# Kernel optimization log

Measured on AMD Instinct MI355X. Metric: run time of the kernel, lower is better.

## Reference

```python
import jax, jax.numpy as jnp
import numpy as np

B, S, DIM = 4, 2048, 1024
HEADS, HD = 16, DIM // 16
HIDDEN, LEVELS = 4 * DIM, 3
LN_EPS = 1e-5


def setup_inputs() -> dict:
    key = jax.random.key(0)
    ks = jax.random.split(key, 10)
    w = lambda k, shape: (jax.random.normal(k, shape, jnp.float32) * 0.02)
    return {
        "x": jax.random.normal(ks[0], (B, S, DIM), jnp.float32),
        "Wq": w(ks[1], (DIM, DIM)),
        "Wk": w(ks[2], (DIM, DIM)),
        "Wv": w(ks[3], (DIM, DIM)),
        "Wo": w(ks[4], (DIM, DIM)),
        "ln1_g": jnp.ones((DIM,), jnp.float32),
        "ln1_b": jnp.zeros((DIM,), jnp.float32),
        "ln2_g": jnp.ones((DIM,), jnp.float32),
        "ln2_b": jnp.zeros((DIM,), jnp.float32),
        "cms_w1": w(ks[5], (LEVELS, DIM, HIDDEN)),
        "cms_b1": jnp.zeros((LEVELS, HIDDEN), jnp.float32),
        "cms_w2": w(ks[6], (LEVELS, HIDDEN, DIM)),
        "cms_b2": jnp.zeros((LEVELS, DIM), jnp.float32),
    }


def _layer_norm(x, g, b):
    m = jnp.mean(x, axis=-1, keepdims=True)
    v = jnp.var(x, axis=-1, keepdims=True)
    return (x - m) * jax.lax.rsqrt(v + LN_EPS) * g + b


def _linear_attn(h, Wq, Wk, Wv, Wo):
    # h: [B, S, DIM]; feature_map(z) = elu(z) + 1 applied to Q and K
    fm = lambda z: jax.nn.elu(z) + 1.0
    Q = fm(h @ Wq).reshape(B, S, HEADS, HD)
    K = fm(h @ Wk).reshape(B, S, HEADS, HD)
    V = (h @ Wv).reshape(B, S, HEADS, HD)
    # scan over time with fast-weight memory M_t = M_{t-1} + k_t (x) v_t
    Qs = jnp.moveaxis(Q, 1, 0)  # [S, B, H, D]
    Ks = jnp.moveaxis(K, 1, 0)
    Vs = jnp.moveaxis(V, 1, 0)

    def step(carry, qkv):
        mem, ksum = carry  # [B,H,D,D], [B,H,D]
        q, k, v = qkv      # each [B,H,D]
        mem = mem + k[..., :, None] * v[..., None, :]
        ksum = ksum + k
        num = jnp.einsum('bhde,bhd->bhe', mem, q)
        den = jnp.einsum('bhd,bhd->bh', ksum, q)[..., None] + 1e-6
        return (mem, ksum), num / den

    init = (jnp.zeros((B, HEADS, HD, HD), h.dtype),
            jnp.zeros((B, HEADS, HD), h.dtype))
    _, ys = jax.lax.scan(step, init, (Qs, Ks, Vs))  # ys: [S,B,H,D]
    out = jnp.moveaxis(ys, 0, 1).reshape(B, S, DIM)
    return out @ Wo


def _cms(h, w1, b1, w2, b2):
    # Continuum Memory System: chain of LEVELS MLPs (dim->4dim->dim).
    y = h
    for l in range(LEVELS):
        y = jax.nn.gelu(y @ w1[l] + b1[l]) @ w2[l] + b2[l]
    return y


def reference(x, Wq, Wk, Wv, Wo, ln1_g, ln1_b, ln2_g, ln2_b,
              cms_w1, cms_b1, cms_w2, cms_b2):
    x = x + _linear_attn(_layer_norm(x, ln1_g, ln1_b), Wq, Wk, Wv, Wo)
    x = x + _cms(_layer_norm(x, ln2_g, ln2_b), cms_w1, cms_b1, cms_w2, cms_b2)
    return x
```

## Files before the change

kernel.cpp:

```cpp
#include <hip/hip_runtime.h>
#include <stdint.h>
#include <math.h>

#define DIM     1024
#define HID     4096
#define SEQ     2048
#define NB      4
#define NH      16
#define HD      64
#define NCHUNK  32
#define MROWS   8192
#define QSTR    3072

typedef unsigned short ushort_t;
typedef __attribute__((ext_vector_type(8))) short bf16x8;
typedef __attribute__((ext_vector_type(4))) float f32x4;

#define OFF_H    ((size_t)0)
#define OFF_Q    ((size_t)16777216)
#define OFF_P    ((size_t)67108864)
#define OFF_KS   ((size_t)100663296)
#define OFF_X1   ((size_t)101187584)
#define OFF_WQT  ((size_t)134742016)
#define OFF_WOT  ((size_t)141033472)
#define OFF_W1T  ((size_t)143130624)
#define OFF_W2T  ((size_t)168296448)
#define OFF_HIDB OFF_Q + 16777216

__device__ __forceinline__ float b2f(ushort_t u) {
    return __uint_as_float(((unsigned int)u) << 16);
}
__device__ __forceinline__ ushort_t f2b(float f) {
    unsigned int u = __float_as_uint(f);
    u += 0x7FFFu + ((u >> 16) & 1u);
    return (ushort_t)(u >> 16);
}
__device__ __forceinline__ void unpack4(uint2 u, float* f) {
    f[0] = __uint_as_float(u.x << 16);
    f[1] = __uint_as_float(u.x & 0xffff0000u);
    f[2] = __uint_as_float(u.y << 16);
    f[3] = __uint_as_float(u.y & 0xffff0000u);
}
__device__ __forceinline__ float fast_gelu(float x) {
    const float u = x * (1.5957691216057308f + 0.07135481627f * x * x);
    const float e = exp2f(-1.4426950408889634f * u);
    return x * __builtin_amdgcn_rcpf(1.0f + e);
}
__device__ __forceinline__ float fast_elu1(float x) {
    return x > 0.0f ? x + 1.0f : exp2f(1.4426950408889634f * x);
}
__device__ __forceinline__ void ldg16(const ushort_t* g, ushort_t* l) {
    __builtin_amdgcn_global_load_lds(
        (const __attribute__((address_space(1))) void*)g,
        (__attribute__((address_space(3))) void*)l, 16, 0, 0);
}

__global__ void __launch_bounds__(256)
transpose_f32_bf16(const float* __restrict__ src, ushort_t* __restrict__ dst, int R, int C)
{
    __shared__ float t[32][33];
    const int bx = blockIdx.x * 32;
    const int by = blockIdx.y * 32;
    const int tx = threadIdx.x, ty = threadIdx.y;
    #pragma unroll
    for (int i = ty; i < 32; i += 8)
        t[i][tx] = src[(size_t)(by + i) * C + bx + tx];
    __syncthreads();
    #pragma unroll
    for (int i = ty; i < 32; i += 8)
        dst[(size_t)(bx + i) * R + by + tx] = f2b(t[tx][i]);
}

__global__ void __launch_bounds__(256)
ln_fwd(const float* __restrict__ xin, const float* __restrict__ g,
       const float* __restrict__ be, ushort_t* __restrict__ out)
{
    const int row = blockIdx.x, tid = threadIdx.x;
    const float4 f = ((const float4*)(xin + (size_t)row * DIM))[tid];
    float v[4] = {f.x, f.y, f.z, f.w};
    float s  = v[0] + v[1] + v[2] + v[3];
    float ss = v[0]*v[0] + v[1]*v[1] + v[2]*v[2] + v[3]*v[3];
    #pragma unroll
    for (int off = 32; off; off >>= 1) {
        s  += __shfl_down(s, off);
        ss += __shfl_down(ss, off);
    }
    __shared__ float red[2][4];
    const int wave = tid >> 6, lane = tid & 63;
    if (lane == 0) { red[0][wave] = s; red[1][wave] = ss; }
    __syncthreads();
    s  = red[0][0] + red[0][1] + red[0][2] + red[0][3];
    ss = red[1][0] + red[1][1] + red[1][2] + red[1][3];
    const float mean = s * (1.0f / DIM);
    const float var  = ss * (1.0f / DIM) - mean * mean;
    const float rstd = rsqrtf(var + 1e-5f);
    ushort_t o[4];
    #pragma unroll
    for (int i = 0; i < 4; i++) {
        const int col = tid * 4 + i;
        o[i] = f2b((v[i] - mean) * rstd * g[col] + be[col]);
    }
    uint2 u2;
    u2.x = (unsigned int)o[0] | ((unsigned int)o[1] << 16);
    u2.y = (unsigned int)o[2] | ((unsigned int)o[3] << 16);
    *(uint2*)(out + (size_t)row * DIM + tid * 4) = u2;
}

#define ACT_NONE 0
#define ACT_ELU1 1
#define ACT_GELU 2
#define ACT_QKV  3

template<int ACT, bool BIAS, bool RES, bool OUTF32>
__global__ void __launch_bounds__(256, 4)
gemm_bt(const ushort_t* __restrict__ A, const ushort_t* __restrict__ Bt,
        const float* __restrict__ bias, const float* __restrict__ resid,
        void* __restrict__ Cout, int M, int N, int K)
{
    __shared__ __align__(16) ushort_t As[2][128 * 32];
    __shared__ __align__(16) ushort_t Bs[2][128 * 32];
    const int tid  = threadIdx.x;
    const int wave = tid >> 6, lane = tid & 63;
    const int bm = blockIdx.x * 128, bn = blockIdx.y * 128;
    const int wm = (wave >> 1) * 64, wn = (wave & 1) * 64;
    const int srow = tid >> 2;
    const int skp  = (tid & 3) * 8;
    const int mrow = lane & 15, kq = (lane >> 4) * 8;
    const bool qkv_elu = (bn < 2048);

    f32x4 acc[4][4] = {};

    const size_t arow0 = (size_t)(bm + srow)      * K;
    const size_t arow1 = (size_t)(bm + srow + 64) * K;
    const size_t brow0 = (size_t)(bn + srow)      * K;
    const size_t brow1 = (size_t)(bn + srow + 64) * K;

    for (int kt = 0; kt < K; kt += 64) {
        __syncthreads();
        #pragma unroll
        for (int hh = 0; hh < 2; hh++) {
            const int ko = kt + hh * 32;
            ldg16(A  + arow0 + ko + skp, As[hh] + tid * 8);
            ldg16(A  + arow1 + ko + skp, As[hh] + 2048 + tid * 8);
            ldg16(Bt + brow0 + ko + skp, Bs[hh] + tid * 8);
            ldg16(Bt + brow1 + ko + skp, Bs[hh] + 2048 + tid * 8);
        }
        __syncthreads();
        #pragma unroll
        for (int hh = 0; hh < 2; hh++) {
            bf16x8 af[4], bfr[4];
            #pragma unroll
            for (int r = 0; r < 4; r++)
                af[r] = *(const bf16x8*)(As[hh] + (wm + r * 16 + mrow) * 32 + kq);
            #pragma unroll
            for (int c = 0; c < 4; c++)
                bfr[c] = *(const bf16x8*)(Bs[hh] + (wn + c * 16 + mrow) * 32 + kq);
            #pragma unroll
            for (int r = 0; r < 4; r++)
                #pragma unroll
                for (int c = 0; c < 4; c++)
                    acc[r][c] = __builtin_amdgcn_mfma_f32_16x16x32_bf16(af[r], bfr[c], acc[r][c], 0, 0, 0);
        }
    }

    const int cr = (lane >> 4) * 4;
    const int cc = lane & 15;
    #pragma unroll
    for (int r = 0; r < 4; r++) {
        #pragma unroll
        for (int c = 0; c < 4; c++) {
            const int gc = bn + wn + c * 16 + cc;
            const float bv = BIAS ? bias[gc] : 0.0f;
            #pragma unroll
            for (int j = 0; j < 4; j++) {
                const int gr = bm + wm + r * 16 + cr + j;
                float vv = acc[r][c][j] + bv;
                if (ACT == ACT_ELU1) vv = fast_elu1(vv);
                if (ACT == ACT_GELU) vv = fast_gelu(vv);
                if (ACT == ACT_QKV)  vv = qkv_elu ? fast_elu1(vv) : vv;
                const size_t oidx = (size_t)gr * N + gc;
                if (RES) vv += resid[oidx];
                if (OUTF32) ((float*)Cout)[oidx] = vv;
                else        ((ushort_t*)Cout)[oidx] = f2b(vv);
            }
        }
    }
}

__global__ void __launch_bounds__(256)
attn_phase1(const ushort_t* __restrict__ qkv,
            float* __restrict__ P, float* __restrict__ Ksum)
{
    const int c = blockIdx.x, h = blockIdx.y, b = blockIdx.z;
    __shared__ ushort_t Ks[64][68], Vs[64][68];
    const int tid = threadIdx.x;
    const size_t rowbase = (size_t)b * SEQ + c * 64;
    #pragma unroll
    for (int i = 0; i < 4; i++) {
        const int lin = tid + 256 * i;
        const int t = lin >> 4, d4 = (lin & 15) * 4;
        const size_t gidx = (rowbase + t) * QSTR + h * HD + d4;
        *(uint2*)&Ks[t][d4] = *(const uint2*)(qkv + 1024 + gidx);
        *(uint2*)&Vs[t][d4] = *(const uint2*)(qkv + 2048 + gidx);
    }
    __syncthreads();
    const int d0 = (tid >> 4) * 4, e0 = (tid & 15) * 4;
    float acc[4][4] = {};
    for (int t = 0; t < 64; t++) {
        float kf[4], vf[4];
        unpack4(*(const uint2*)&Ks[t][d0], kf);
        unpack4(*(const uint2*)&Vs[t][e0], vf);
        #pragma unroll
        for (int i = 0; i < 4; i++)
            #pragma unroll
            for (int j = 0; j < 4; j++)
                acc[i][j] += kf[i] * vf[j];
    }
    const size_t pbase = (((size_t)b * NH + h) * NCHUNK + c) * 4096;
    #pragma unroll
    for (int i = 0; i < 4; i++) {
        float4 o; o.x = acc[i][0]; o.y = acc[i][1]; o.z = acc[i][2]; o.w = acc[i][3];
        *(float4*)(P + pbase + (size_t)(d0 + i) * 64 + e0) = o;
    }
    if (tid < 64) {
        float a = 0.0f;
        for (int t = 0; t < 64; t++) a += b2f(Ks[t][tid]);
        Ksum[(((size_t)b * NH + h) * NCHUNK + c) * 64 + tid] = a;
    }
}

__global__ void __launch_bounds__(256)
attn_prefix(float* __restrict__ P, float* __restrict__ Ksum)
{
    const int bh = blockIdx.y;
    const int e  = blockIdx.x * 256 + threadIdx.x;
    const size_t base = (size_t)bh * NCHUNK * 4096 + e;
    float acc = 0.0f;
    #pragma unroll
    for (int c = 0; c < NCHUNK; c++) {
        const float t = P[base + (size_t)c * 4096];
        P[base + (size_t)c * 4096] = acc;
        acc += t;
    }
    if (blockIdx.x == 0 && threadIdx.x < 64) {
        const size_t kb = (size_t)bh * NCHUNK * 64 + threadIdx.x;
        float a = 0.0f;
        #pragma unroll
        for (int c = 0; c < NCHUNK; c++) {
            const float t = Ksum[kb + c * 64];
            Ksum[kb + c * 64] = a;
            a += t;
        }
    }
}

__global__ void __launch_bounds__(256)
attn_phase2(const ushort_t* __restrict__ qkv, const float* __restrict__ P,
            const float* __restrict__ Ksum, ushort_t* __restrict__ Out)
{
    const int c = blockIdx.x, h = blockIdx.y, b = blockIdx.z;
    const int tid = threadIdx.x;
    __shared__ ushort_t Qs[64][68], KsB[64][68], VsB[64][68];
    __shared__ float S[64][68];
    __shared__ float Mp[64][64];
    __shared__ float kp[64];
    __shared__ float partial[4][64];
    const size_t rowbase = (size_t)b * SEQ + c * 64;
    const size_t pbase = (((size_t)b * NH + h) * NCHUNK + c) * 4096;
    #pragma unroll
    for (int i = 0; i < 4; i++) {
        const int lin = tid + 256 * i;
        const int t = lin >> 4, d4 = (lin & 15) * 4;
        const size_t gidx = (rowbase + t) * QSTR + h * HD + d4;
        *(uint2*)&Qs[t][d4]  = *(const uint2*)(qkv + gidx);
        *(uint2*)&KsB[t][d4] = *(const uint2*)(qkv + 1024 + gidx);
        *(uint2*)&VsB[t][d4] = *(const uint2*)(qkv + 2048 + gidx);
        *(float4*)&Mp[t][d4] = *(const float4*)(P + pbase + lin * 4);
    }
    if (tid < 64) kp[tid] = Ksum[(((size_t)b * NH + h) * NCHUNK + c) * 64 + tid];
    __syncthreads();

    const int t0 = (tid >> 4) * 4;
    const int c0 = (tid & 15) * 4;

    {
        float accS[4][4] = {};
        for (int d4 = 0; d4 < 64; d4 += 4) {
            float qf[4][4], kf[4][4];
            #pragma unroll
            for (int i = 0; i < 4; i++) {
                unpack4(*(const uint2*)&Qs[t0 + i][d4], qf[i]);
                unpack4(*(const uint2*)&KsB[c0 + i][d4], kf[i]);
            }
            #pragma unroll
            for (int i = 0; i < 4; i++)
                #pragma unroll
                for (int j = 0; j < 4; j++)
                    #pragma unroll
                    for (int dd = 0; dd < 4; dd++)
                        accS[i][j] += qf[i][dd] * kf[j][dd];
        }
        #pragma unroll
        for (int i = 0; i < 4; i++) {
            float4 sv;
            sv.x = (c0 + 0 <= t0 + i) ? accS[i][0] : 0.0f;
            sv.y = (c0 + 1 <= t0 + i) ? accS[i][1] : 0.0f;
            sv.z = (c0 + 2 <= t0 + i) ? accS[i][2] : 0.0f;
            sv.w = (c0 + 3 <= t0 + i) ? accS[i][3] : 0.0f;
            *(float4*)&S[t0 + i][c0] = sv;
        }
    }
    __syncthreads();

    {
        const int t = tid & 63, q = tid >> 6;
        const int base = q * 16;
        float a = 0.0f;
        #pragma unroll
        for (int ii = 0; ii < 16; ii++) a += S[t][base + ii];
        #pragma unroll
        for (int d = 0; d < 16; d++) a += b2f(Qs[t][base + d]) * kp[base + d];
        partial[q][t] = a;
    }
    __syncthreads();

    float acc[4][4] = {};
    for (int ii = 0; ii < 64; ii++) {
        float vf[4];
        unpack4(*(const uint2*)&VsB[ii][c0], vf);
        #pragma unroll
        for (int i = 0; i < 4; i++) {
            const float s = S[t0 + i][ii];
            #pragma unroll
            for (int j = 0; j < 4; j++) acc[i][j] += s * vf[j];
        }
    }
    for (int d = 0; d < 64; d++) {
        const float4 mp = *(const float4*)&Mp[d][c0];
        #pragma unroll
        for (int i = 0; i < 4; i++) {
            const float qv = b2f(Qs[t0 + i][d]);
            acc[i][0] += qv * mp.x; acc[i][1] += qv * mp.y;
            acc[i][2] += qv * mp.z; acc[i][3] += qv * mp.w;
        }
    }
    #pragma unroll
    for (int i = 0; i < 4; i++) {
        const float dent = partial[0][t0 + i] + partial[1][t0 + i] +
                           partial[2][t0 + i] + partial[3][t0 + i] + 1e-6f;
        const float r = 1.0f / dent;
        ushort_t o[4];
        #pragma unroll
        for (int j = 0; j < 4; j++) o[j] = f2b(acc[i][j] * r);
        uint2 u2;
        u2.x = (unsigned int)o[0] | ((unsigned int)o[1] << 16);
        u2.y = (unsigned int)o[2] | ((unsigned int)o[3] << 16);
        *(uint2*)(Out + (rowbase + t0 + i) * DIM + h * HD + c0) = u2;
    }
}

extern "C" void kernel_launch(void* const* d_in, const int* in_sizes, int n_in,
                              void* d_out, int out_size, void* d_ws, size_t ws_size,
                              hipStream_t stream)
{
    const float* x      = (const float*)d_in[0];
    const float* Wq     = (const float*)d_in[1];
    const float* Wk     = (const float*)d_in[2];
    const float* Wv     = (const float*)d_in[3];
    const float* Wo     = (const float*)d_in[4];
    const float* ln1g   = (const float*)d_in[5];
    const float* ln1b   = (const float*)d_in[6];
    const float* ln2g   = (const float*)d_in[7];
    const float* ln2b   = (const float*)d_in[8];
    const float* cw1    = (const float*)d_in[9];
    const float* cb1    = (const float*)d_in[10];
    const float* cw2    = (const float*)d_in[11];
    const float* cb2    = (const float*)d_in[12];

    char* ws = (char*)d_ws;
    ushort_t* h     = (ushort_t*)(ws + OFF_H);
    ushort_t* qkv   = (ushort_t*)(ws + OFF_Q);
    float*    Pb    = (float*)(ws + OFF_P);
    float*    ksb   = (float*)(ws + OFF_KS);
    float*    x1    = (float*)(ws + OFF_X1);
    ushort_t* wqkvt = (ushort_t*)(ws + OFF_WQT);
    ushort_t* wot   = (ushort_t*)(ws + OFF_WOT);
    ushort_t* w1t   = (ushort_t*)(ws + OFF_W1T);
    ushort_t* w2t   = (ushort_t*)(ws + OFF_W2T);
    ushort_t* hid   = (ushort_t*)(ws + OFF_HIDB);
    float*    outp  = (float*)d_out;

    const dim3 tb(32, 8);
    transpose_f32_bf16<<<dim3(32, 32), tb, 0, stream>>>(Wq, wqkvt,                   DIM, DIM);
    transpose_f32_bf16<<<dim3(32, 32), tb, 0, stream>>>(Wk, wqkvt + 1024 * 1024,     DIM, DIM);
    transpose_f32_bf16<<<dim3(32, 32), tb, 0, stream>>>(Wv, wqkvt + 2 * 1024 * 1024, DIM, DIM);
    transpose_f32_bf16<<<dim3(32, 32), tb, 0, stream>>>(Wo, wot, DIM, DIM);
    for (int l = 0; l < 3; l++) {
        transpose_f32_bf16<<<dim3(128, 32), tb, 0, stream>>>(cw1 + (size_t)l * DIM * HID,
                                                             w1t + (size_t)l * HID * DIM, DIM, HID);
        transpose_f32_bf16<<<dim3(32, 128), tb, 0, stream>>>(cw2 + (size_t)l * HID * DIM,
                                                             w2t + (size_t)l * DIM * HID, HID, DIM);
    }

    ln_fwd<<<MROWS, 256, 0, stream>>>(x, ln1g, ln1b, h);

    gemm_bt<ACT_QKV, false, false, false><<<dim3(64, 24), 256, 0, stream>>>(
        h, wqkvt, nullptr, nullptr, qkv, MROWS, QSTR, DIM);

    attn_phase1<<<dim3(NCHUNK, NH, NB), 256, 0, stream>>>(qkv, Pb, ksb);
    attn_prefix<<<dim3(16, 64), 256, 0, stream>>>(Pb, ksb);
    attn_phase2<<<dim3(NCHUNK, NH, NB), 256, 0, stream>>>(qkv, Pb, ksb, h);

    gemm_bt<ACT_NONE, false, true, true><<<dim3(64, 8), 256, 0, stream>>>(h, wot, nullptr, x, x1, MROWS, DIM, DIM);

    ln_fwd<<<MROWS, 256, 0, stream>>>(x1, ln2g, ln2b, h);

    const ushort_t* cur = h;
    for (int l = 0; l < 3; l++) {
        gemm_bt<ACT_GELU, true, false, false><<<dim3(64, 32), 256, 0, stream>>>(
            cur, w1t + (size_t)l * HID * DIM, cb1 + (size_t)l * HID, nullptr, hid, MROWS, HID, DIM);
        if (l < 2) {
            gemm_bt<ACT_NONE, true, false, false><<<dim3(64, 8), 256, 0, stream>>>(
                hid, w2t + (size_t)l * DIM * HID, cb2 + (size_t)l * DIM, nullptr, h, MROWS, DIM, HID);
            cur = h;
        } else {
            gemm_bt<ACT_NONE, true, true, true><<<dim3(64, 8), 256, 0, stream>>>(
                hid, w2t + (size_t)l * DIM * HID, cb2 + (size_t)l * DIM, x1, outp, MROWS, DIM, HID);
        }
    }
    (void)in_sizes; (void)n_in; (void)out_size; (void)ws_size;
}
```

Baseline: 883.2 us.

## Replace 128x128 GEMM with 256-row 8-wave pipelined GEMM using swizzled LDS

Adds a new gemm256 kernel that uses 256xBN tiles, 512 threads (8 waves), and an XOR-swizzled LDS layout to avoid bank conflicts. It double-buffers global-to-LDS loads across sub-phases, interleaving stages with MFMA groups under explicit barriers and s_setprio. All GEMM launches in the transformer block are switched to it, with BN=256 for the wide FFN up-projection. This aims to raise arithmetic intensity and overlap memory with compute. The cost is much higher LDS use and register pressure, plus fewer blocks for the narrow N=1024 GEMMs (256 blocks), which may underfill the GPU.

```diff
diff --git a/kernel.cpp b/kernel.cpp
--- a/kernel.cpp
+++ b/kernel.cpp
@@ -123,13 +123,12 @@
     const int wave = tid >> 6, lane = tid & 63;
     const int bm = blockIdx.x * 128, bn = blockIdx.y * 128;
     const int wm = (wave >> 1) * 64, wn = (wave & 1) * 64;
+    const int skp  = (tid & 3) * 8;
     const int srow = tid >> 2;
-    const int skp  = (tid & 3) * 8;
     const int mrow = lane & 15, kq = (lane >> 4) * 8;
     const bool qkv_elu = (bn < 2048);
 
     f32x4 acc[4][4] = {};
-
     const size_t arow0 = (size_t)(bm + srow)      * K;
     const size_t arow1 = (size_t)(bm + srow + 64) * K;
     const size_t brow0 = (size_t)(bn + srow)      * K;
@@ -162,7 +161,6 @@
                     acc[r][c] = __builtin_amdgcn_mfma_f32_16x16x32_bf16(af[r], bfr[c], acc[r][c], 0, 0, 0);
         }
     }
-
     const int cr = (lane >> 4) * 4;
     const int cc = lane & 15;
     #pragma unroll
@@ -185,6 +183,158 @@
             }
         }
     }
+}
+
+
+#define G256_RD_A(BUF, FR0) \
+    _Pragma("unroll") for (int _i = 0; _i < 4; ++_i) \
+    _Pragma("unroll") for (int _kk = 0; _kk < 2; ++_kk) \
+        af[_i][_kk] = *(const bf16x8*)(ldsb + (BUF) + aoff + (((FR0) + _i) << 11) \
+                                       + (((_kk << 6) | qv16) ^ mflip))
+
+#define G256_RD_B(BUF, FC0, CNT) \
+    _Pragma("unroll") for (int _c = 0; _c < (CNT); ++_c) \
+    _Pragma("unroll") for (int _kk = 0; _kk < 2; ++_kk) \
+        bf[(FC0) + _c][_kk] = *(const bf16x8*)(ldsb + (BUF) + boff + (((FC0) + _c) << 11) \
+                                               + (((_kk << 6) | qv16) ^ mflip))
+
+#define G256_MFMA(AR, C0, CNT) \
+    _Pragma("unroll") for (int _i = 0; _i < 4; ++_i) \
+    _Pragma("unroll") for (int _c = 0; _c < (CNT); ++_c) \
+    _Pragma("unroll") for (int _kk = 0; _kk < 2; ++_kk) \
+        acc[(AR) + _i][(C0) + _c] = __builtin_amdgcn_mfma_f32_16x16x32_bf16( \
+            af[_i][_kk], bf[(C0) + _c][_kk], acc[(AR) + _i][(C0) + _c], 0, 0, 0)
+
+#define G256_STAGE_A(T, H) do { \
+    char* _d = ldsb + (((T) & 1) ? (int)BUFSZ : 0) + ((H) << 14) + (tid << 4); \
+    const ushort_t* _s = pA + (size_t)((H) * 128) * K + (size_t)(T) * 64; \
+    ldg16(_s, (ushort_t*)_d); \
+    ldg16(_s + (size_t)64 * K, (ushort_t*)(_d + 8192)); \
+} while (0)
+
+#define G256_STAGE_B(T, H) do { \
+    char* _d = ldsb + (((T) & 1) ? (int)BUFSZ : 0) + 32768 + (H) * (BN_ * 64) + (tid << 4); \
+    const ushort_t* _s = pB + (size_t)((H) * (BN_ >> 1)) * K + (size_t)(T) * 64; \
+    ldg16(_s, (ushort_t*)_d); \
+    if (BN_ == 256) ldg16(_s + (size_t)64 * K, (ushort_t*)(_d + 8192)); \
+} while (0)
+
+#define G256_BARW() do { \
+    __builtin_amdgcn_s_barrier(); \
+    asm volatile("s_waitcnt lgkmcnt(0)" ::: "memory"); \
+    __builtin_amdgcn_sched_barrier(0); \
+    __builtin_amdgcn_s_setprio(1); \
+} while (0)
+
+#define G256_ENDP() do { \
+    __builtin_amdgcn_s_setprio(0); \
+    __builtin_amdgcn_s_barrier(); \
+} while (0)
+
+template<int BN_, int ACT, bool BIAS, bool RES, bool OUTF32>
+__global__ void __launch_bounds__(512, 2)
+gemm256(const ushort_t* __restrict__ A, const ushort_t* __restrict__ Bt,
+        const float* __restrict__ bias, const float* __restrict__ resid,
+        void* __restrict__ Cout, int M, int N, int K)
+{
+    constexpr int NF    = BN_ / 64;
+    constexpr int BUFSZ = 32768 + BN_ * 128;
+    __shared__ __align__(16) char ldsb[2 * BUFSZ];
+
+    const int tid  = threadIdx.x;
+    const int lane = tid & 63, wave = tid >> 6;
+    const int wm_idx = wave >> 2, wn_idx = wave & 3;
+    const int bm = blockIdx.x * 256, bn = blockIdx.y * BN_;
+
+    const int r0  = tid >> 3;
+    const int kbs = ((tid & 7) << 4) ^ ((r0 & 1) << 6);
+    const ushort_t* pA = A  + (size_t)(bm + r0) * K + (kbs >> 1);
+    const ushort_t* pB = Bt + (size_t)(bn + r0) * K + (kbs >> 1);
+
+    const int m     = lane & 15;
+    const int qv16  = (lane >> 4) << 4;
+    const int mflip = (m & 1) << 6;
+    const int aoff  = (wm_idx * 128 + m) << 7;
+    const int boff  = 32768 + ((wn_idx * (BN_ >> 2) + m) << 7);
+
+    f32x4  acc[8][NF] = {};
+    bf16x8 af[4][2], bf[NF][2];
+
+    const int NT    = K >> 6;
+    const int niter = NT >> 1;
+
+    G256_STAGE_A(0, 0); G256_STAGE_A(0, 1);
+    G256_STAGE_B(0, 0); G256_STAGE_B(0, 1);
+    G256_STAGE_A(1, 0);
+    asm volatile("s_waitcnt vmcnt(2)" ::: "memory");
+    __builtin_amdgcn_s_barrier();
+
+    for (int it = 0; it < niter; ++it) {
+        const int  t    = it << 1;
+        const bool more = (it + 1) < niter;
+
+        G256_RD_A(0, 0); G256_RD_B(0, 0, NF / 2);
+        G256_STAGE_A(t + 1, 1);
+        G256_BARW(); G256_MFMA(0, 0, NF / 2); G256_ENDP();
+
+        G256_RD_B(0, NF / 2, NF / 2);
+        G256_STAGE_B(t + 1, 0);
+        G256_BARW(); G256_MFMA(0, NF / 2, NF / 2); G256_ENDP();
+
+        G256_RD_A(0, 4);
+        G256_STAGE_B(t + 1, 1);
+        G256_BARW(); G256_MFMA(4, 0, NF / 2); G256_ENDP();
+
+        if (more) G256_STAGE_A(t + 2, 0);
+        G256_BARW(); G256_MFMA(4, NF / 2, NF / 2);
+        __builtin_amdgcn_s_setprio(0);
+        if (more) asm volatile("s_waitcnt vmcnt(2)" ::: "memory");
+        else      asm volatile("s_waitcnt vmcnt(0)" ::: "memory");
+        __builtin_amdgcn_s_barrier();
+
+        G256_RD_A(BUFSZ, 0); G256_RD_B(BUFSZ, 0, NF / 2);
+        if (more) G256_STAGE_A(t + 2, 1);
+        G256_BARW(); G256_MFMA(0, 0, NF / 2); G256_ENDP();
+
+        G256_RD_B(BUFSZ, NF / 2, NF / 2);
+        if (more) G256_STAGE_B(t + 2, 0);
+        G256_BARW(); G256_MFMA(0, NF / 2, NF / 2); G256_ENDP();
+
+        G256_RD_A(BUFSZ, 4);
+        if (more) G256_STAGE_B(t + 2, 1);
+        G256_BARW(); G256_MFMA(4, 0, NF / 2); G256_ENDP();
+
+        if (more) G256_STAGE_A(t + 3, 0);
+        G256_BARW(); G256_MFMA(4, NF / 2, NF / 2);
+        __builtin_amdgcn_s_setprio(0);
+        if (more) asm volatile("s_waitcnt vmcnt(2)" ::: "memory");
+        else      asm volatile("s_waitcnt vmcnt(0)" ::: "memory");
+        __builtin_amdgcn_s_barrier();
+    }
+
+    const int cr   = (lane >> 4) << 2;
+    const int ccol = lane & 15;
+    #pragma unroll
+    for (int fr = 0; fr < 8; ++fr) {
+        #pragma unroll
+        for (int fc = 0; fc < NF; ++fc) {
+            const int gc = bn + wn_idx * (BN_ >> 2) + fc * 16 + ccol;
+            const float bv = BIAS ? bias[gc] : 0.0f;
+            #pragma unroll
+            for (int j = 0; j < 4; ++j) {
+                const int gr = bm + wm_idx * 128 + fr * 16 + cr + j;
+                float vv = acc[fr][fc][j] + bv;
+                if (ACT == ACT_ELU1) vv = fast_elu1(vv);
+                if (ACT == ACT_GELU) vv = fast_gelu(vv);
+                if (ACT == ACT_QKV)  vv = (bn < 2048) ? fast_elu1(vv) : vv;
+                const size_t oidx = (size_t)gr * N + gc;
+                if (RES) vv += resid[oidx];
+                if (OUTF32) ((float*)Cout)[oidx] = vv;
+                else        ((ushort_t*)Cout)[oidx] = f2b(vv);
+            }
+        }
+    }
+    (void)M;
 }
 
 __global__ void __launch_bounds__(256)
@@ -404,27 +554,28 @@
 
     ln_fwd<<<MROWS, 256, 0, stream>>>(x, ln1g, ln1b, h);
 
-    gemm_bt<ACT_QKV, false, false, false><<<dim3(64, 24), 256, 0, stream>>>(
+    gemm256<128, ACT_QKV, false, false, false><<<dim3(32, 24), 512, 0, stream>>>(
         h, wqkvt, nullptr, nullptr, qkv, MROWS, QSTR, DIM);
 
     attn_phase1<<<dim3(NCHUNK, NH, NB), 256, 0, stream>>>(qkv, Pb, ksb);
     attn_prefix<<<dim3(16, 64), 256, 0, stream>>>(Pb, ksb);
     attn_phase2<<<dim3(NCHUNK, NH, NB), 256, 0, stream>>>(qkv, Pb, ksb, h);
 
-    gemm_bt<ACT_NONE, false, true, true><<<dim3(64, 8), 256, 0, stream>>>(h, wot, nullptr, x, x1, MROWS, DIM, DIM);
+    gemm256<128, ACT_NONE, false, true, true><<<dim3(32, 8), 512, 0, stream>>>(
+        h, wot, nullptr, x, x1, MROWS, DIM, DIM);
 
     ln_fwd<<<MROWS, 256, 0, stream>>>(x1, ln2g, ln2b, h);
 
     const ushort_t* cur = h;
     for (int l = 0; l < 3; l++) {
-        gemm_bt<ACT_GELU, true, false, false><<<dim3(64, 32), 256, 0, stream>>>(
+        gemm256<256, ACT_GELU, true, false, false><<<dim3(32, 16), 512, 0, stream>>>(
             cur, w1t + (size_t)l * HID * DIM, cb1 + (size_t)l * HID, nullptr, hid, MROWS, HID, DIM);
         if (l < 2) {
-            gemm_bt<ACT_NONE, true, false, false><<<dim3(64, 8), 256, 0, stream>>>(
+            gemm256<128, ACT_NONE, true, false, false><<<dim3(32, 8), 512, 0, stream>>>(
                 hid, w2t + (size_t)l * DIM * HID, cb2 + (size_t)l * DIM, nullptr, h, MROWS, DIM, HID);
             cur = h;
         } else {
-            gemm_bt<ACT_NONE, true, true, true><<<dim3(64, 8), 256, 0, stream>>>(
+            gemm256<128, ACT_NONE, true, true, true><<<dim3(32, 8), 512, 0, stream>>>(
                 hid, w2t + (size_t)l * DIM * HID, cb2 + (size_t)l * DIM, x1, outp, MROWS, DIM, HID);
         }
     }
```

Measured after the change: 1.067 ms. +20.8%, slower.
